# Performance work log

Hardware: AMD Instinct MI355X
Metric: run time of the kernel (lower is better)

## Reference

```python
import jax, jax.numpy as jnp
import numpy as np

EMBED = 1024
HEADS = 16
DK = EMBED // HEADS


def setup_inputs() -> dict:
    key = jax.random.key(0)
    ks = jax.random.split(key, 6)
    B, S = 2, 2048
    scale = 1.0 / np.sqrt(EMBED)
    x = jax.random.normal(ks[0], (B, S, EMBED), dtype=jnp.float32)
    Wq = jax.random.normal(ks[1], (EMBED, EMBED), dtype=jnp.float32) * scale
    Wk = jax.random.normal(ks[2], (EMBED, EMBED), dtype=jnp.float32) * scale
    Wv = jax.random.normal(ks[3], (EMBED, EMBED), dtype=jnp.float32) * scale
    Wo = jax.random.normal(ks[4], (EMBED, EMBED), dtype=jnp.float32) * scale
    qw = jnp.zeros((HEADS, 1), dtype=jnp.float32)  # quantum_weight, init quantum_scale=0
    return {"x": x, "Wq": Wq, "Wk": Wk, "Wv": Wv, "Wo": Wo, "qw": qw}


def reference(x, Wq, Wk, Wv, Wo, qw):
    B, S, E = x.shape
    # nn.Linear with no bias: y = x @ W.T; split heads -> [B,H,S,Dk]
    def proj(W):
        return (x @ W.T).reshape(B, S, HEADS, DK).transpose(0, 2, 1, 3)
    q, k, v = proj(Wq), proj(Wk), proj(Wv)
    scores = jnp.einsum('bhsd,bhtd->bhst', q, k) / np.sqrt(DK)
    attn = jax.nn.softmax(scores, axis=-1)  # dropout in eval mode: identity
    classical = jnp.einsum('bhst,bhtd->bhsd', attn, v)
    w = jax.nn.sigmoid(qw)[:, :, None]  # [H,1,1] per-head mixing weight
    out = w * jnp.sin(classical) + (1.0 - w) * classical
    out = out.transpose(0, 2, 1, 3).reshape(B, S, E)
    return out @ Wo.T
```

## Files before the change

### kernel.cpp

```cpp
#include <hip/hip_runtime.h>
#include <math.h>

constexpr int Ec  = 1024;
constexpr int Hc  = 16;
constexpr int DKc = 64;
constexpr int Bc  = 2;
constexpr int Sc  = 2048;
constexpr int Mc  = Bc * Sc;

typedef _Float16 half8 __attribute__((ext_vector_type(8)));
typedef _Float16 half4 __attribute__((ext_vector_type(4)));
typedef float    floatx4 __attribute__((ext_vector_type(4)));

#define MFMA16(a, b, c) __builtin_amdgcn_mfma_f32_16x16x32_f16(a, b, c, 0, 0, 0)

__device__ __forceinline__ void async_lds16(const _Float16* g, _Float16* l)
{
    __builtin_amdgcn_global_load_lds(
        (const __attribute__((address_space(1))) unsigned int*)g,
        (__attribute__((address_space(3))) unsigned int*)l, 16, 0, 0);
}

__global__ __launch_bounds__(256)
void convert_to_h(const float4* __restrict__ x,
                  const float4* __restrict__ wq,
                  const float4* __restrict__ wk,
                  const float4* __restrict__ wv,
                  const float4* __restrict__ wo,
                  half4* __restrict__ dst)
{
    const int i = blockIdx.x * 256 + threadIdx.x;
    const float4* src; int off;
    if      (i < 1048576) { src = x;  off = i; }
    else if (i < 1310720) { src = wq; off = i - 1048576; }
    else if (i < 1572864) { src = wk; off = i - 1310720; }
    else if (i < 1835008) { src = wv; off = i - 1572864; }
    else                  { src = wo; off = i - 1835008; }
    const float4 v = src[off];
    half4 o;
    o.x = (_Float16)v.x; o.y = (_Float16)v.y;
    o.z = (_Float16)v.z; o.w = (_Float16)v.w;
    dst[i] = o;
}

__device__ __forceinline__ void mfma_gemm_core(const _Float16* __restrict__ A,
                                               const _Float16* __restrict__ Bw,
                                               int m0, int n0,
                                               _Float16* As, _Float16* Bs,
                                               floatx4 acc[4][4])
{
    const int tid  = threadIdx.x;
    const int wave = tid >> 6, lane = tid & 63;
    const int l16  = lane & 15, quad = lane >> 4;
    const int wrow = (wave >> 1) * 64, wcol = (wave & 1) * 64;

    const int srow = wave * 32 + (lane >> 2);
    const int kseg = (lane & 3) * 8;
    const _Float16* ga = A  + (size_t)(m0 + srow) * Ec + kseg;
    const _Float16* gb = Bw + (size_t)(n0 + srow) * Ec + kseg;
    _Float16* lA = As + wave * 1024;
    _Float16* lB = Bs + wave * 1024;

    for (int kt = 0; kt < Ec; kt += 32) {
        async_lds16(ga,             lA);
        async_lds16(ga + 16 * Ec,   lA + 512);
        async_lds16(gb,             lB);
        async_lds16(gb + 16 * Ec,   lB + 512);
        ga += 32; gb += 32;
        __syncthreads();

        half8 af[4], bf[4];
#pragma unroll
        for (int i = 0; i < 4; ++i)
            af[i] = *(const half8*)&As[(wrow + i * 16 + l16) * 32 + quad * 8];
#pragma unroll
        for (int j = 0; j < 4; ++j)
            bf[j] = *(const half8*)&Bs[(wcol + j * 16 + l16) * 32 + quad * 8];
#pragma unroll
        for (int i = 0; i < 4; ++i)
#pragma unroll
            for (int j = 0; j < 4; ++j)
                acc[i][j] = MFMA16(af[i], bf[j], acc[i][j]);
        __syncthreads();
    }
}

__global__ __launch_bounds__(256)
void gemm_qkv_mfma(const _Float16* __restrict__ xh,
                   const _Float16* __restrict__ wqh,
                   const _Float16* __restrict__ wkh,
                   const _Float16* __restrict__ wvh,
                   _Float16* __restrict__ Qh,
                   _Float16* __restrict__ Kh,
                   _Float16* __restrict__ VTh)
{
    __shared__ __align__(16) _Float16 As[128 * 32];
    __shared__ __align__(16) _Float16 Bs[128 * 32];
    const int z = blockIdx.z;
    const _Float16* W = (z == 0) ? wqh : (z == 1) ? wkh : wvh;
    const int m0 = blockIdx.y * 128, n0 = blockIdx.x * 128;

    floatx4 acc[4][4] = {};
    mfma_gemm_core(xh, W, m0, n0, As, Bs, acc);

    const int tid  = threadIdx.x;
    const int wave = tid >> 6, lane = tid & 63;
    const int l16  = lane & 15, quad = lane >> 4;
    const int wrow = (wave >> 1) * 64, wcol = (wave & 1) * 64;

    if (z == 2) {
#pragma unroll
        for (int i = 0; i < 4; ++i)
#pragma unroll
            for (int j = 0; j < 4; ++j) {
                const int n = n0 + wcol + j * 16 + l16;
                const int h = n >> 6, d = n & 63;
#pragma unroll
                for (int r = 0; r < 4; ++r) {
                    const int m = m0 + wrow + i * 16 + quad * 4 + r;
                    const int b = m >> 11, s = m & (Sc - 1);
                    VTh[((size_t)((b * Hc + h) * DKc + d)) * Sc + s] =
                        (_Float16)acc[i][j][r];
                }
            }
    } else {
        _Float16* out = (z == 0) ? Qh : Kh;
        const float scale = (z == 0) ? 0.125f : 1.0f;
#pragma unroll
        for (int i = 0; i < 4; ++i)
#pragma unroll
            for (int j = 0; j < 4; ++j) {
                const int n = n0 + wcol + j * 16 + l16;
#pragma unroll
                for (int r = 0; r < 4; ++r) {
                    const int m = m0 + wrow + i * 16 + quad * 4 + r;
                    out[(size_t)m * Ec + n] = (_Float16)(acc[i][j][r] * scale);
                }
            }
    }
}

__global__ __launch_bounds__(256)
void gemm_out_mfma(const _Float16* __restrict__ A,
                   const _Float16* __restrict__ W,
                   float* __restrict__ C)
{
    __shared__ __align__(16) _Float16 As[128 * 32];
    __shared__ __align__(16) _Float16 Bs[128 * 32];
    const int m0 = blockIdx.y * 128, n0 = blockIdx.x * 128;

    floatx4 acc[4][4] = {};
    mfma_gemm_core(A, W, m0, n0, As, Bs, acc);

    const int tid  = threadIdx.x;
    const int wave = tid >> 6, lane = tid & 63;
    const int l16  = lane & 15, quad = lane >> 4;
    const int wrow = (wave >> 1) * 64, wcol = (wave & 1) * 64;
#pragma unroll
    for (int i = 0; i < 4; ++i)
#pragma unroll
        for (int j = 0; j < 4; ++j) {
            const int n = n0 + wcol + j * 16 + l16;
#pragma unroll
            for (int r = 0; r < 4; ++r) {
                const int m = m0 + wrow + i * 16 + quad * 4 + r;
                C[(size_t)m * Ec + n] = acc[i][j][r];
            }
        }
}

__global__ __launch_bounds__(256)
void flash_attn(const _Float16* __restrict__ Qh,
                const _Float16* __restrict__ Kh,
                const _Float16* __restrict__ VTh,
                const float* __restrict__ qw,
                _Float16* __restrict__ Mixh)
{
    constexpr int BM = 128, BN = 64, LDH = 72;
    __shared__ _Float16 Kt[BN][LDH];
    __shared__ _Float16 Vt[DKc][LDH];
    __shared__ _Float16 Ps[BM][LDH];

    const int tid  = threadIdx.x;
    const int wave = tid >> 6, lane = tid & 63;
    const int quad = lane >> 4, l16 = lane & 15;
    const int q0 = blockIdx.x * BM;
    const int bh = blockIdx.y;
    const int h  = bh & (Hc - 1), b = bh >> 4;

    half8 aq[2][2];
#pragma unroll
    for (int u = 0; u < 2; ++u) {
        const _Float16* qp = Qh + (size_t)(b * Sc + q0 + wave * 32 + u * 16 + l16) * Ec
                                + h * DKc + quad * 8;
        aq[u][0] = *(const half8*)qp;
        aq[u][1] = *(const half8*)(qp + 32);
    }

    const int srow = tid >> 2;
    const int sseg = (tid & 3) * 16;
    const _Float16* Kg = Kh + (size_t)(b * Sc + srow) * Ec + h * DKc + sseg;
    const _Float16* Vg = VTh + ((size_t)(bh * DKc + srow)) * Sc + sseg;

    half8 kr0 = *(const half8*)Kg, kr1 = *(const half8*)(Kg + 8);
    half8 vr0 = *(const half8*)Vg, vr1 = *(const half8*)(Vg + 8);
    Kg += (size_t)BN * Ec; Vg += BN;
    *(half8*)&Kt[srow][sseg]     = kr0;
    *(half8*)&Kt[srow][sseg + 8] = kr1;

    floatx4 o[2][4] = {};
    float l_run[2][4] = {};

    for (int n = 0; n < Sc / BN; ++n) {
        __syncthreads();
        *(half8*)&Vt[srow][sseg]     = vr0;
        *(half8*)&Vt[srow][sseg + 8] = vr1;
        const bool more = (n + 1 < Sc / BN);
        if (more) {
            kr0 = *(const half8*)Kg; kr1 = *(const half8*)(Kg + 8);
            vr0 = *(const half8*)Vg; vr1 = *(const half8*)(Vg + 8);
            Kg += (size_t)BN * Ec; Vg += BN;
        }

        floatx4 s[2][4];
#pragma unroll
        for (int i = 0; i < 4; ++i) {
            const half8 bk0 = *(const half8*)&Kt[i * 16 + l16][quad * 8];
            const half8 bk1 = *(const half8*)&Kt[i * 16 + l16][32 + quad * 8];
            const floatx4 z = {0.f, 0.f, 0.f, 0.f};
            s[0][i] = MFMA16(aq[0][1], bk1, MFMA16(aq[0][0], bk0, z));
            s[1][i] = MFMA16(aq[1][1], bk1, MFMA16(aq[1][0], bk0, z));
        }

#pragma unroll
        for (int u = 0; u < 2; ++u) {
            const int prow = wave * 32 + u * 16 + quad * 4;
#pragma unroll
            for (int i = 0; i < 4; ++i) {
                const float p0 = __expf(s[u][i][0]);
                const float p1 = __expf(s[u][i][1]);
                const float p2 = __expf(s[u][i][2]);
                const float p3 = __expf(s[u][i][3]);
                l_run[u][0] += p0; l_run[u][1] += p1;
                l_run[u][2] += p2; l_run[u][3] += p3;
                Ps[prow + 0][i * 16 + l16] = (_Float16)p0;
                Ps[prow + 1][i * 16 + l16] = (_Float16)p1;
                Ps[prow + 2][i * 16 + l16] = (_Float16)p2;
                Ps[prow + 3][i * 16 + l16] = (_Float16)p3;
            }
        }
        __syncthreads();

        half8 ap[2][2];
#pragma unroll
        for (int u = 0; u < 2; ++u) {
            const _Float16* pp = &Ps[wave * 32 + u * 16 + l16][quad * 8];
            ap[u][0] = *(const half8*)pp;
            ap[u][1] = *(const half8*)(pp + 32);
        }
#pragma unroll
        for (int jd = 0; jd < 4; ++jd) {
            const half8 bv0 = *(const half8*)&Vt[jd * 16 + l16][quad * 8];
            const half8 bv1 = *(const half8*)&Vt[jd * 16 + l16][32 + quad * 8];
#pragma unroll
            for (int u = 0; u < 2; ++u) {
                o[u][jd] = MFMA16(ap[u][0], bv0, o[u][jd]);
                o[u][jd] = MFMA16(ap[u][1], bv1, o[u][jd]);
            }
        }

        if (more) {
            *(half8*)&Kt[srow][sseg]     = kr0;
            *(half8*)&Kt[srow][sseg + 8] = kr1;
        }
    }

    const float wmix = 1.f / (1.f + __expf(-qw[h]));
#pragma unroll
    for (int u = 0; u < 2; ++u)
#pragma unroll
        for (int r = 0; r < 4; ++r) {
            float l = l_run[u][r];
            l += __shfl_xor(l, 1); l += __shfl_xor(l, 2);
            l += __shfl_xor(l, 4); l += __shfl_xor(l, 8);
            const float inv = 1.f / l;
            const int m = q0 + wave * 32 + u * 16 + quad * 4 + r;
            _Float16* mp = Mixh + (size_t)(b * Sc + m) * Ec + h * DKc;
#pragma unroll
            for (int jd = 0; jd < 4; ++jd) {
                const float v = o[u][jd][r] * inv;
                mp[jd * 16 + l16] = (_Float16)(wmix * __sinf(v) + (1.f - wmix) * v);
            }
        }
}

extern "C" void kernel_launch(void* const* d_in, const int* in_sizes, int n_in,
                              void* d_out, int out_size, void* d_ws, size_t ws_size,
                              hipStream_t stream)
{
    const float* x  = (const float*)d_in[0];
    const float* Wq = (const float*)d_in[1];
    const float* Wk = (const float*)d_in[2];
    const float* Wv = (const float*)d_in[3];
    const float* Wo = (const float*)d_in[4];
    const float* qw = (const float*)d_in[5];
    float* out = (float*)d_out;

    _Float16* hb   = (_Float16*)d_ws;
    _Float16* xh   = hb;
    _Float16* wqh  = hb + (size_t)4 * 1024 * 1024;
    _Float16* wkh  = hb + (size_t)5 * 1024 * 1024;
    _Float16* wvh  = hb + (size_t)6 * 1024 * 1024;
    _Float16* woh  = hb + (size_t)7 * 1024 * 1024;
    _Float16* Qh   = hb + (size_t)8 * 1024 * 1024;
    _Float16* Kh   = hb + (size_t)12 * 1024 * 1024;
    _Float16* VTh  = hb + (size_t)16 * 1024 * 1024;
    _Float16* mixh = hb + (size_t)20 * 1024 * 1024;

    convert_to_h<<<dim3(8192), dim3(256), 0, stream>>>(
        (const float4*)x, (const float4*)Wq, (const float4*)Wk,
        (const float4*)Wv, (const float4*)Wo, (half4*)hb);

    gemm_qkv_mfma<<<dim3(Ec / 128, Mc / 128, 3), dim3(256), 0, stream>>>(
        xh, wqh, wkh, wvh, Qh, Kh, VTh);

    flash_attn<<<dim3(Sc / 128, Bc * Hc), dim3(256), 0, stream>>>(
        Qh, Kh, VTh, qw, mixh);

    gemm_out_mfma<<<dim3(Ec / 128, Mc / 128), dim3(256), 0, stream>>>(
        mixh, woh, out);
}
```

Before: 217.9 us.

## Transpose attention score MFMA and narrow output GEMM tile to 128x64

In flash attention the QK^T MFMA operands are swapped, so each lane holds four consecutive keys for one query row. This lets P be written to LDS as one packed half4 store instead of four scalar stores, and keeps a single running row sum per lane instead of four. The final row-sum reduction is adjusted to match, using cross-quad shuffles plus a broadcast shuffle. Separately, the output GEMM now uses 128x64 tiles with its own inline async-LDS loop, doubling the block count to fill more CUs. The cost is that each block reuses loaded A data across fewer output columns.

```diff
diff --git a/kernel.cpp b/kernel.cpp
--- a/kernel.cpp
+++ b/kernel.cpp
@@ -146,20 +146,48 @@
                    float* __restrict__ C)
 {
     __shared__ __align__(16) _Float16 As[128 * 32];
-    __shared__ __align__(16) _Float16 Bs[128 * 32];
-    const int m0 = blockIdx.y * 128, n0 = blockIdx.x * 128;
-
-    floatx4 acc[4][4] = {};
-    mfma_gemm_core(A, W, m0, n0, As, Bs, acc);
+    __shared__ __align__(16) _Float16 Bs[64 * 32];
+    const int m0 = blockIdx.y * 128, n0 = blockIdx.x * 64;
 
     const int tid  = threadIdx.x;
     const int wave = tid >> 6, lane = tid & 63;
     const int l16  = lane & 15, quad = lane >> 4;
-    const int wrow = (wave >> 1) * 64, wcol = (wave & 1) * 64;
+    const int wrow = (wave >> 1) * 64, wcol = (wave & 1) * 32;
+
+    const int kseg = (lane & 3) * 8;
+    const _Float16* ga = A + (size_t)(m0 + wave * 32 + (lane >> 2)) * Ec + kseg;
+    const _Float16* gb = W + (size_t)(n0 + wave * 16 + (lane >> 2)) * Ec + kseg;
+    _Float16* lA = As + wave * 1024;
+    _Float16* lB = Bs + wave * 512;
+
+    floatx4 acc[4][2] = {};
+
+    for (int kt = 0; kt < Ec; kt += 32) {
+        async_lds16(ga,           lA);
+        async_lds16(ga + 16 * Ec, lA + 512);
+        async_lds16(gb,           lB);
+        ga += 32; gb += 32;
+        __syncthreads();
+
+        half8 af[4], bf[2];
+#pragma unroll
+        for (int i = 0; i < 4; ++i)
+            af[i] = *(const half8*)&As[(wrow + i * 16 + l16) * 32 + quad * 8];
+#pragma unroll
+        for (int j = 0; j < 2; ++j)
+            bf[j] = *(const half8*)&Bs[(wcol + j * 16 + l16) * 32 + quad * 8];
+#pragma unroll
+        for (int i = 0; i < 4; ++i)
+#pragma unroll
+            for (int j = 0; j < 2; ++j)
+                acc[i][j] = MFMA16(af[i], bf[j], acc[i][j]);
+        __syncthreads();
+    }
+
 #pragma unroll
     for (int i = 0; i < 4; ++i)
 #pragma unroll
-        for (int j = 0; j < 4; ++j) {
+        for (int j = 0; j < 2; ++j) {
             const int n = n0 + wcol + j * 16 + l16;
 #pragma unroll
             for (int r = 0; r < 4; ++r) {
@@ -209,7 +237,7 @@
     *(half8*)&Kt[srow][sseg + 8] = kr1;
 
     floatx4 o[2][4] = {};
-    float l_run[2][4] = {};
+    float l_run[2] = {0.f, 0.f};
 
     for (int n = 0; n < Sc / BN; ++n) {
         __syncthreads();
@@ -222,31 +250,30 @@
             Kg += (size_t)BN * Ec; Vg += BN;
         }
 
-        floatx4 s[2][4];
+        floatx4 st[2][4];
 #pragma unroll
         for (int i = 0; i < 4; ++i) {
-            const half8 bk0 = *(const half8*)&Kt[i * 16 + l16][quad * 8];
-            const half8 bk1 = *(const half8*)&Kt[i * 16 + l16][32 + quad * 8];
+            const half8 ak0 = *(const half8*)&Kt[i * 16 + l16][quad * 8];
+            const half8 ak1 = *(const half8*)&Kt[i * 16 + l16][32 + quad * 8];
             const floatx4 z = {0.f, 0.f, 0.f, 0.f};
-            s[0][i] = MFMA16(aq[0][1], bk1, MFMA16(aq[0][0], bk0, z));
-            s[1][i] = MFMA16(aq[1][1], bk1, MFMA16(aq[1][0], bk0, z));
+            st[0][i] = MFMA16(ak1, aq[0][1], MFMA16(ak0, aq[0][0], z));
+            st[1][i] = MFMA16(ak1, aq[1][1], MFMA16(ak0, aq[1][0], z));
         }
 
 #pragma unroll
         for (int u = 0; u < 2; ++u) {
-            const int prow = wave * 32 + u * 16 + quad * 4;
+            const int prow = wave * 32 + u * 16 + l16;
 #pragma unroll
             for (int i = 0; i < 4; ++i) {
-                const float p0 = __expf(s[u][i][0]);
-                const float p1 = __expf(s[u][i][1]);
-                const float p2 = __expf(s[u][i][2]);
-                const float p3 = __expf(s[u][i][3]);
-                l_run[u][0] += p0; l_run[u][1] += p1;
-                l_run[u][2] += p2; l_run[u][3] += p3;
-                Ps[prow + 0][i * 16 + l16] = (_Float16)p0;
-                Ps[prow + 1][i * 16 + l16] = (_Float16)p1;
-                Ps[prow + 2][i * 16 + l16] = (_Float16)p2;
-                Ps[prow + 3][i * 16 + l16] = (_Float16)p3;
+                const float p0 = __expf(st[u][i][0]);
+                const float p1 = __expf(st[u][i][1]);
+                const float p2 = __expf(st[u][i][2]);
+                const float p3 = __expf(st[u][i][3]);
+                l_run[u] += (p0 + p1) + (p2 + p3);
+                half4 pk;
+                pk.x = (_Float16)p0; pk.y = (_Float16)p1;
+                pk.z = (_Float16)p2; pk.w = (_Float16)p3;
+                *(half4*)&Ps[prow][i * 16 + quad * 4] = pk;
             }
         }
         __syncthreads();
@@ -277,12 +304,15 @@
 
     const float wmix = 1.f / (1.f + __expf(-qw[h]));
 #pragma unroll
+    for (int u = 0; u < 2; ++u) {
+        l_run[u] += __shfl_xor(l_run[u], 16);
+        l_run[u] += __shfl_xor(l_run[u], 32);
+    }
+#pragma unroll
     for (int u = 0; u < 2; ++u)
 #pragma unroll
         for (int r = 0; r < 4; ++r) {
-            float l = l_run[u][r];
-            l += __shfl_xor(l, 1); l += __shfl_xor(l, 2);
-            l += __shfl_xor(l, 4); l += __shfl_xor(l, 8);
+            const float l = __shfl(l_run[u], (lane & 48) | (quad * 4 + r));
             const float inv = 1.f / l;
             const int m = q0 + wave * 32 + u * 16 + quad * 4 + r;
             _Float16* mp = Mixh + (size_t)(b * Sc + m) * Ec + h * DKc;
@@ -327,6 +357,6 @@
     flash_attn<<<dim3(Sc / 128, Bc * Hc), dim3(256), 0, stream>>>(
         Qh, Kh, VTh, qw, mixh);
 
-    gemm_out_mfma<<<dim3(Ec / 128, Mc / 128), dim3(256), 0, stream>>>(
+    gemm_out_mfma<<<dim3(Ec / 64, Mc / 128), dim3(256), 0, stream>>>(
         mixh, woh, out);
 }
```

Measured after the change: 202.9 us. 1.07x faster.
